# Optimization experiments

Hardware: AMD Instinct MI355X
Metric: run time of the kernel (lower is better)

Reference implementation:

```python
import jax, jax.numpy as jnp
import numpy as np
from jax import lax

B, T, D_IN = 512, 256, 64
N_NEURONS, D_STATE, D_OUT = 2048, 64, 10


def setup_inputs() -> dict:
    key = jax.random.key(0)
    k_seq, k_enc, k_bias, k_gain, k_sd, k_d = jax.random.split(key, 6)
    enc = jax.random.normal(k_enc, (N_NEURONS, D_IN + D_STATE), dtype=jnp.float32)
    # hypersphere strategy: unit-norm encoder rows
    enc = enc / jnp.linalg.norm(enc, axis=-1, keepdims=True)
    return {
        "seq": jax.random.normal(k_seq, (B, T, D_IN), dtype=jnp.float32),
        "encoders": enc,
        "bias": jax.random.normal(k_bias, (N_NEURONS,), dtype=jnp.float32),
        "gain": jax.random.uniform(k_gain, (N_NEURONS,), dtype=jnp.float32),
        "state_decoders": jax.random.normal(k_sd, (N_NEURONS, D_STATE), dtype=jnp.float32) * 0.02,
        "decoders": jax.random.normal(k_d, (N_NEURONS, D_OUT), dtype=jnp.float32) * 0.02,
    }


def reference(seq, encoders, bias, gain, state_decoders, decoders):
    # seq: (B, T, d_in). Recurrent decode-then-re-encode loop over T.
    b = seq.shape[0]
    d_state = state_decoders.shape[1]
    n = encoders.shape[0]

    def step(carry, u_t):
        s, _ = carry  # s: (B, d_state)
        x_aug = jnp.concatenate([u_t, s], axis=-1)  # (B, d_in + d_state)
        a = jnp.abs(gain * (x_aug @ encoders.T) + bias)  # (B, n_neurons), activation='abs'
        s_new = a @ state_decoders  # (B, d_state)
        return (s_new, a), None

    s0 = jnp.zeros((b, d_state), dtype=seq.dtype)
    a0 = jnp.zeros((b, n), dtype=seq.dtype)
    (_, a_final), _ = lax.scan(step, (s0, a0), jnp.swapaxes(seq, 0, 1))
    return a_final @ decoders  # (B, d_out)
```

## Files before the change

kernel.cpp:

```cpp
#include <hip/hip_runtime.h>
#include <math.h>

#define B_    512
#define T_    256
#define DIN   64
#define DS    64
#define KK    128
#define NN    2048
#define DOUT  10

#define NT      512
#define BT      8
#define NTILES  (NN / NT)
#define BTILES  (B_ / BT)
#define THREADS 512
#define NWG     (NTILES * BTILES)

#define PS1        ((size_t)BTILES * NTILES * BT * DS)
#define PS_TOT     (2 * PS1)
#define ETSW_OFF   PS_TOT
#define ETSW_F16   ((size_t)KK * NN)
#define SDSW_OFF   (ETSW_OFF + ETSW_F16 / 2)
#define SDSW_F16   ((size_t)NN * DS)
#define BAR_OFF    (SDSW_OFF + SDSW_F16 / 2)
#define BAR_UINTS  4096

typedef _Float16 half8 __attribute__((ext_vector_type(8)));
typedef float    f32x4 __attribute__((ext_vector_type(4)));

__global__ __launch_bounds__(256) void pre_kernel(const float* __restrict__ enc,
                                                  const float* __restrict__ sd,
                                                  float* __restrict__ ws,
                                                  float* __restrict__ out) {
    size_t i = (size_t)blockIdx.x * blockDim.x + threadIdx.x;
    size_t stride = (size_t)gridDim.x * blockDim.x;
    unsigned int* bar = (unsigned int*)(ws + BAR_OFF);
    for (size_t x = i; x < BAR_UINTS; x += stride) bar[x] = 0u;
    _Float16* EtSw = (_Float16*)(ws + ETSW_OFF);
    for (size_t x = i; x < (size_t)KK * NN; x += stride) {
        const int j     = (int)(x & 7);
        const int lane  = (int)((x >> 3) & 63);
        const int ktile = (int)((x >> 9) & 3);
        const int ntile = (int)((x >> 11) & 3);
        const int w     = (int)((x >> 13) & 7);
        const int nt    = (int)(x >> 16);
        const int n = nt * 512 + w * 64 + ntile * 16 + (lane & 15);
        const int k = ktile * 32 + ((lane >> 4) << 3) + j;
        EtSw[x] = (_Float16)enc[(size_t)n * KK + k];
    }
    _Float16* SdSw = (_Float16*)(ws + SDSW_OFF);
    for (size_t x = i; x < (size_t)NN * DS; x += stride) {
        const int j     = (int)(x & 7);
        const int lane  = (int)((x >> 3) & 63);
        const int ktile = (int)((x >> 9) & 7);
        const int kh    = (int)((x >> 12) & 1);
        const int cg    = (int)((x >> 13) & 3);
        const int nt    = (int)(x >> 15);
        const int n = nt * 512 + kh * 256 + ktile * 32 + ((lane >> 4) << 3) + j;
        const int c = cg * 16 + (lane & 15);
        SdSw[x] = (_Float16)sd[(size_t)n * DS + c];
    }
    for (size_t x = i; x < (size_t)B_ * DOUT; x += stride) out[x] = 0.0f;
}

__global__ __launch_bounds__(THREADS, 2) void persist_kernel(
    const float* __restrict__ seq,
    const _Float16* __restrict__ EtSw,
    const _Float16* __restrict__ SdSw,
    const float* __restrict__ bias,
    const float* __restrict__ gain,
    const float* __restrict__ dec,
    float* __restrict__ ps,
    unsigned int* __restrict__ bar,
    float* __restrict__ out)
{
    __shared__ _Float16 xh[16][136];
    __shared__ _Float16 Ash[16][520];
    __shared__ float Dp[4][8][17];

    const int tid = threadIdx.x;
    const int nt = blockIdx.x & (NTILES - 1);
    const int bt = blockIdx.x >> 2;
    const int n0 = nt * NT;
    const int b0 = bt * BT;

    unsigned int* cnt = bar + (size_t)bt * 32;

    const int w = tid >> 6;
    const int l = tid & 63;
    const int rs = tid >> 6;
    const int cs = tid & 63;
    const int m16 = l & 15;
    const int q8  = (l >> 4) << 3;
    const int cg  = w & 3;
    const int kh  = w >> 2;

    const _Float16* EtW = EtSw + ((size_t)(nt * 8 + w) << 13);
    const _Float16* SdW = SdSw + ((size_t)((nt * 4 + cg) * 2 + kh) << 12);

    half8 etf[4][4];
    #pragma unroll
    for (int n4 = 0; n4 < 4; ++n4)
        #pragma unroll
        for (int kt = 0; kt < 4; ++kt)
            etf[n4][kt] = *(const half8*)&EtW[(n4 << 11) + (kt << 9) + (size_t)l * 8];
    half8 sdf[8];
    #pragma unroll
    for (int kt = 0; kt < 8; ++kt)
        sdf[kt] = *(const half8*)&SdW[(kt << 9) + (size_t)l * 8];

    float gv[4], bv[4];
    #pragma unroll
    for (int n4 = 0; n4 < 4; ++n4) {
        gv[n4] = gain[n0 + w * 64 + n4 * 16 + m16];
        bv[n4] = bias[n0 + w * 64 + n4 * 16 + m16];
    }

    {
        unsigned int* xz = (unsigned int*)&xh[0][0];
        for (int i2 = tid; i2 < 16 * 136 / 2; i2 += THREADS) xz[i2] = 0u;
    }
    __syncthreads();

    for (int t = 0; t < T_; ++t) {
        if (tid < 128) {
            const int r = tid >> 4, c = (tid & 15) << 2;
            const float4 uv = *(const float4*)&seq[((size_t)(b0 + r) * T_ + t) * DIN + c];
            _Float16* p = &xh[r][c];
            p[0] = (_Float16)uv.x; p[1] = (_Float16)uv.y;
            p[2] = (_Float16)uv.z; p[3] = (_Float16)uv.w;
        }
        __syncthreads();

        f32x4 acc[4];
        #pragma unroll
        for (int n4 = 0; n4 < 4; ++n4) acc[n4] = (f32x4){0.f, 0.f, 0.f, 0.f};
        {
            const half8 af0 = *(const half8*)&xh[m16][q8];
            const half8 af1 = *(const half8*)&xh[m16][32 + q8];
            #pragma unroll
            for (int n4 = 0; n4 < 4; ++n4) {
                acc[n4] = __builtin_amdgcn_mfma_f32_16x16x32_f16(af0, etf[n4][0], acc[n4], 0, 0, 0);
                acc[n4] = __builtin_amdgcn_mfma_f32_16x16x32_f16(af1, etf[n4][1], acc[n4], 0, 0, 0);
            }
        }

        if (t > 0) {
            if (tid == 0) {
                while (__hip_atomic_load(cnt, __ATOMIC_RELAXED, __HIP_MEMORY_SCOPE_AGENT)
                       < 4u * (unsigned)t)
                    __builtin_amdgcn_s_sleep(1);
            }
            __syncthreads();
            const float* pb = ps + (size_t)((t - 1) & 1) * PS1;
            float ssum = 0.f;
            #pragma unroll
            for (int p = 0; p < NTILES; ++p)
                ssum += __hip_atomic_load(
                    pb + (((size_t)bt * NTILES + p) * BT + rs) * DS + cs,
                    __ATOMIC_RELAXED, __HIP_MEMORY_SCOPE_AGENT);
            xh[rs][DIN + cs] = (_Float16)ssum;
        } else {
            xh[rs][DIN + cs] = (_Float16)0.f;
        }
        __syncthreads();

        {
            const half8 af2 = *(const half8*)&xh[m16][64 + q8];
            const half8 af3 = *(const half8*)&xh[m16][96 + q8];
            #pragma unroll
            for (int n4 = 0; n4 < 4; ++n4) {
                acc[n4] = __builtin_amdgcn_mfma_f32_16x16x32_f16(af2, etf[n4][2], acc[n4], 0, 0, 0);
                acc[n4] = __builtin_amdgcn_mfma_f32_16x16x32_f16(af3, etf[n4][3], acc[n4], 0, 0, 0);
            }
        }

        if (l < 32) {
            const int rq = (l >> 4) << 2;
            #pragma unroll
            for (int n4 = 0; n4 < 4; ++n4) {
                const int n = w * 64 + n4 * 16 + m16;
                Ash[rq + 0][n] = (_Float16)fabsf(gv[n4] * acc[n4][0] + bv[n4]);
                Ash[rq + 1][n] = (_Float16)fabsf(gv[n4] * acc[n4][1] + bv[n4]);
                Ash[rq + 2][n] = (_Float16)fabsf(gv[n4] * acc[n4][2] + bv[n4]);
                Ash[rq + 3][n] = (_Float16)fabsf(gv[n4] * acc[n4][3] + bv[n4]);
            }
        }
        __syncthreads();

        if (t == T_ - 1) {
            for (int idx = tid; idx < BT * DOUT; idx += THREADS) {
                const int r = idx / DOUT;
                const int d = idx % DOUT;
                float o = 0.f;
                #pragma unroll 8
                for (int n = 0; n < NT; ++n)
                    o += (float)Ash[r][n] * dec[(size_t)(n0 + n) * DOUT + d];
                atomicAdd(&out[(size_t)(b0 + r) * DOUT + d], o);
            }
            return;
        }

        {
            f32x4 d0 = (f32x4){0.f, 0.f, 0.f, 0.f};
            f32x4 d1 = (f32x4){0.f, 0.f, 0.f, 0.f};
            #pragma unroll
            for (int kt = 0; kt < 8; kt += 2) {
                const half8 a0 = *(const half8*)&Ash[m16][kh * 256 + kt * 32 + q8];
                d0 = __builtin_amdgcn_mfma_f32_16x16x32_f16(a0, sdf[kt], d0, 0, 0, 0);
                const half8 a1 = *(const half8*)&Ash[m16][kh * 256 + (kt + 1) * 32 + q8];
                d1 = __builtin_amdgcn_mfma_f32_16x16x32_f16(a1, sdf[kt + 1], d1, 0, 0, 0);
            }
            d0[0] += d1[0]; d0[1] += d1[1]; d0[2] += d1[2]; d0[3] += d1[3];
            if (kh == 1 && l < 32) {
                const int rq = (l >> 4) << 2;
                Dp[cg][rq + 0][m16] = d0[0];
                Dp[cg][rq + 1][m16] = d0[1];
                Dp[cg][rq + 2][m16] = d0[2];
                Dp[cg][rq + 3][m16] = d0[3];
            }
            __syncthreads();
            if (kh == 0 && l < 32) {
                const int rq = (l >> 4) << 2;
                float* pw = ps + (size_t)(t & 1) * PS1
                               + (((size_t)bt * NTILES + nt) * BT) * DS + 16 * cg + m16;
                #pragma unroll
                for (int r = 0; r < 4; ++r) {
                    const float v = d0[r] + Dp[cg][rq + r][m16];
                    __hip_atomic_store(pw + (size_t)(rq + r) * DS, v,
                                       __ATOMIC_RELAXED, __HIP_MEMORY_SCOPE_AGENT);
                }
            }
        }

        asm volatile("s_waitcnt vmcnt(0)" ::: "memory");
        __syncthreads();
        if (tid == 0)
            __hip_atomic_fetch_add(cnt, 1u, __ATOMIC_RELAXED, __HIP_MEMORY_SCOPE_AGENT);
    }
}

extern "C" void kernel_launch(void* const* d_in, const int* in_sizes, int n_in,
                              void* d_out, int out_size, void* d_ws, size_t ws_size,
                              hipStream_t stream) {
    const float* seq  = (const float*)d_in[0];
    const float* enc  = (const float*)d_in[1];
    const float* bias = (const float*)d_in[2];
    const float* gain = (const float*)d_in[3];
    const float* sd   = (const float*)d_in[4];
    const float* dec  = (const float*)d_in[5];
    float* out = (float*)d_out;
    float* ws  = (float*)d_ws;

    pre_kernel<<<dim3(1024), dim3(256), 0, stream>>>(enc, sd, ws, out);

    float* ps = ws;
    const _Float16* EtSw = (const _Float16*)(ws + ETSW_OFF);
    const _Float16* SdSw = (const _Float16*)(ws + SDSW_OFF);
    unsigned int* bar = (unsigned int*)(ws + BAR_OFF);

    persist_kernel<<<dim3(NWG), dim3(THREADS), 0, stream>>>(
        seq, EtSw, SdSw, bias, gain, dec, ps, bar, out);
}
```

Measured before the change: 660.6 us.

## Replace counter barrier with tagged 64-bit partial-state words for per-element sync

Removes the per-batch-tile atomic counter and its spin-wait by packing each partial state value with a timestep tag in a 64-bit word. Each consumer thread spins directly on the four partial words it needs until all carry the expected tag, then sums them. This drops the trailing vmcnt wait, a __syncthreads, the fetch_add, and the single-thread poll followed by a block barrier. In exchange it doubles the partial-buffer size, has every thread poll global memory, and relies on 64-bit atomic stores being observed whole.

```diff
diff --git a/kernel.cpp b/kernel.cpp
--- a/kernel.cpp
+++ b/kernel.cpp
@@ -16,14 +16,12 @@
 #define THREADS 512
 #define NWG     (NTILES * BTILES)
 
-#define PS1        ((size_t)BTILES * NTILES * BT * DS)
-#define PS_TOT     (2 * PS1)
-#define ETSW_OFF   PS_TOT
+#define PSQ_ELEMS  ((size_t)BTILES * NTILES * BT * DS)
+#define PS_FLOATS  (4 * PSQ_ELEMS)
+#define ETSW_OFF   PS_FLOATS
 #define ETSW_F16   ((size_t)KK * NN)
 #define SDSW_OFF   (ETSW_OFF + ETSW_F16 / 2)
 #define SDSW_F16   ((size_t)NN * DS)
-#define BAR_OFF    (SDSW_OFF + SDSW_F16 / 2)
-#define BAR_UINTS  4096
 
 typedef _Float16 half8 __attribute__((ext_vector_type(8)));
 typedef float    f32x4 __attribute__((ext_vector_type(4)));
@@ -34,8 +32,8 @@
                                                   float* __restrict__ out) {
     size_t i = (size_t)blockIdx.x * blockDim.x + threadIdx.x;
     size_t stride = (size_t)gridDim.x * blockDim.x;
-    unsigned int* bar = (unsigned int*)(ws + BAR_OFF);
-    for (size_t x = i; x < BAR_UINTS; x += stride) bar[x] = 0u;
+    unsigned long long* psq = (unsigned long long*)ws;
+    for (size_t x = i; x < 2 * PSQ_ELEMS; x += stride) psq[x] = 0ull;
     _Float16* EtSw = (_Float16*)(ws + ETSW_OFF);
     for (size_t x = i; x < (size_t)KK * NN; x += stride) {
         const int j     = (int)(x & 7);
@@ -70,8 +68,7 @@
     const float* __restrict__ bias,
     const float* __restrict__ gain,
     const float* __restrict__ dec,
-    float* __restrict__ ps,
-    unsigned int* __restrict__ bar,
+    unsigned long long* __restrict__ psq,
     float* __restrict__ out)
 {
     __shared__ _Float16 xh[16][136];
@@ -83,8 +80,6 @@
     const int bt = blockIdx.x >> 2;
     const int n0 = nt * NT;
     const int b0 = bt * BT;
-
-    unsigned int* cnt = bar + (size_t)bt * 32;
 
     const int w = tid >> 6;
     const int l = tid & 63;
@@ -116,6 +111,8 @@
         bv[n4] = bias[n0 + w * 64 + n4 * 16 + m16];
     }
 
+    const size_t fan_base = ((size_t)bt * NTILES) * BT * DS + (size_t)rs * DS + cs;
+
     {
         unsigned int* xz = (unsigned int*)&xh[0][0];
         for (int i2 = tid; i2 < 16 * 136 / 2; i2 += THREADS) xz[i2] = 0u;
@@ -146,19 +143,20 @@
         }
 
         if (t > 0) {
-            if (tid == 0) {
-                while (__hip_atomic_load(cnt, __ATOMIC_RELAXED, __HIP_MEMORY_SCOPE_AGENT)
-                       < 4u * (unsigned)t)
-                    __builtin_amdgcn_s_sleep(1);
-            }
-            __syncthreads();
-            const float* pb = ps + (size_t)((t - 1) & 1) * PS1;
-            float ssum = 0.f;
-            #pragma unroll
-            for (int p = 0; p < NTILES; ++p)
-                ssum += __hip_atomic_load(
-                    pb + (((size_t)bt * NTILES + p) * BT + rs) * DS + cs,
-                    __ATOMIC_RELAXED, __HIP_MEMORY_SCOPE_AGENT);
+            const unsigned long long* pb = psq + (size_t)((t - 1) & 1) * PSQ_ELEMS + fan_base;
+            const unsigned utag = (unsigned)t;
+            unsigned long long v0, v1, v2, v3;
+            for (;;) {
+                v0 = __hip_atomic_load(pb + 0 * (BT * DS), __ATOMIC_RELAXED, __HIP_MEMORY_SCOPE_AGENT);
+                v1 = __hip_atomic_load(pb + 1 * (BT * DS), __ATOMIC_RELAXED, __HIP_MEMORY_SCOPE_AGENT);
+                v2 = __hip_atomic_load(pb + 2 * (BT * DS), __ATOMIC_RELAXED, __HIP_MEMORY_SCOPE_AGENT);
+                v3 = __hip_atomic_load(pb + 3 * (BT * DS), __ATOMIC_RELAXED, __HIP_MEMORY_SCOPE_AGENT);
+                if ((unsigned)(v0 >> 32) == utag && (unsigned)(v1 >> 32) == utag &&
+                    (unsigned)(v2 >> 32) == utag && (unsigned)(v3 >> 32) == utag)
+                    break;
+            }
+            const float ssum = __uint_as_float((unsigned)v0) + __uint_as_float((unsigned)v1)
+                             + __uint_as_float((unsigned)v2) + __uint_as_float((unsigned)v3);
             xh[rs][DIN + cs] = (_Float16)ssum;
         } else {
             xh[rs][DIN + cs] = (_Float16)0.f;
@@ -212,6 +210,7 @@
                 d1 = __builtin_amdgcn_mfma_f32_16x16x32_f16(a1, sdf[kt + 1], d1, 0, 0, 0);
             }
             d0[0] += d1[0]; d0[1] += d1[1]; d0[2] += d1[2]; d0[3] += d1[3];
+
             if (kh == 1 && l < 32) {
                 const int rq = (l >> 4) << 2;
                 Dp[cg][rq + 0][m16] = d0[0];
@@ -220,23 +219,21 @@
                 Dp[cg][rq + 3][m16] = d0[3];
             }
             __syncthreads();
+
             if (kh == 0 && l < 32) {
                 const int rq = (l >> 4) << 2;
-                float* pw = ps + (size_t)(t & 1) * PS1
-                               + (((size_t)bt * NTILES + nt) * BT) * DS + 16 * cg + m16;
+                unsigned long long* pw = psq + (size_t)(t & 1) * PSQ_ELEMS
+                    + (((size_t)bt * NTILES + nt) * BT) * DS + 16 * cg + m16;
+                const unsigned long long tg = (unsigned long long)(unsigned)(t + 1) << 32;
                 #pragma unroll
                 for (int r = 0; r < 4; ++r) {
                     const float v = d0[r] + Dp[cg][rq + r][m16];
-                    __hip_atomic_store(pw + (size_t)(rq + r) * DS, v,
+                    __hip_atomic_store(pw + (size_t)(rq + r) * DS,
+                                       tg | (unsigned long long)__float_as_uint(v),
                                        __ATOMIC_RELAXED, __HIP_MEMORY_SCOPE_AGENT);
                 }
             }
         }
-
-        asm volatile("s_waitcnt vmcnt(0)" ::: "memory");
-        __syncthreads();
-        if (tid == 0)
-            __hip_atomic_fetch_add(cnt, 1u, __ATOMIC_RELAXED, __HIP_MEMORY_SCOPE_AGENT);
     }
 }
 
@@ -254,11 +251,10 @@
 
     pre_kernel<<<dim3(1024), dim3(256), 0, stream>>>(enc, sd, ws, out);
 
-    float* ps = ws;
+    unsigned long long* psq = (unsigned long long*)ws;
     const _Float16* EtSw = (const _Float16*)(ws + ETSW_OFF);
     const _Float16* SdSw = (const _Float16*)(ws + SDSW_OFF);
-    unsigned int* bar = (unsigned int*)(ws + BAR_OFF);
 
     persist_kernel<<<dim3(NWG), dim3(THREADS), 0, stream>>>(
-        seq, EtSw, SdSw, bias, gain, dec, ps, bar, out);
+        seq, EtSw, SdSw, bias, gain, dec, psq, out);
 }
```

Result: faster. 640.9 us (-3.0%).
